# Optimization experiments

Measured on AMD Instinct MI355X. Metric: run time of the kernel, lower is better.

The kernel has to match this reference:

```python
import jax, jax.numpy as jnp
import numpy as np

L = 2        # num_layers
D = 512      # d_model
H = 8        # heads
C = 512      # GAT per-head out channels (= d_model, concat=False -> mean over heads)
B, S, E = 4, 512, 4096
NEG = jnp.float32(-1e9)


def setup_inputs() -> dict:
    key = jax.random.key(0)
    ks = jax.random.split(key, 20)
    sc = 0.02  # weight init scale
    inp = {
        'x': jax.random.normal(ks[0], (B, S, D), jnp.float32),
        'Wq': jax.random.normal(ks[1], (L, D, D), jnp.float32) * sc,
        'bq': jnp.zeros((L, D), jnp.float32),
        'Wk': jax.random.normal(ks[2], (L, D, D), jnp.float32) * sc,
        'bk': jnp.zeros((L, D), jnp.float32),
        'Wv': jax.random.normal(ks[3], (L, D, D), jnp.float32) * sc,
        'bv': jnp.zeros((L, D), jnp.float32),
        'Wo': jax.random.normal(ks[4], (L, D, D), jnp.float32) * sc,
        'bo': jnp.zeros((L, D), jnp.float32),
        'gatW': jax.random.normal(ks[5], (L, D, H * C), jnp.float32) * sc,
        'att_src': jax.random.normal(ks[6], (L, H, C), jnp.float32) * sc,
        'att_dst': jax.random.normal(ks[7], (L, H, C), jnp.float32) * sc,
        'gat_bias': jnp.zeros((L, C), jnp.float32),
        'ln_g': jnp.ones((L, D), jnp.float32),
        'ln_b': jnp.zeros((L, D), jnp.float32),
        'input_len': jax.random.randint(ks[8], (B,), S // 2, S + 1, jnp.int32),
        'edges': jax.random.randint(ks[9], (B, 2, E), 0, S // 2, jnp.int32),
        'edge_num': jax.random.randint(ks[10], (B,), E // 2, E + 1, jnp.int32),
    }
    return inp


def layer_norm(x, g, b, eps=1e-5):
    m = x.mean(-1, keepdims=True)
    v = ((x - m) ** 2).mean(-1, keepdims=True)
    return (x - m) * jax.lax.rsqrt(v + eps) * g + b


def mha(x, pad_mask, Wq, bq, Wk, bk, Wv, bv, Wo, bo):
    # pad_mask: [B,S] True where padded (masked out)
    b, s, d = x.shape
    dh = d // H
    q = (x @ Wq + bq).reshape(b, s, H, dh)
    k = (x @ Wk + bk).reshape(b, s, H, dh)
    v = (x @ Wv + bv).reshape(b, s, H, dh)
    scores = jnp.einsum('bqhd,bkhd->bhqk', q, k) / jnp.float32(np.sqrt(dh))
    scores = jnp.where(pad_mask[:, None, None, :], NEG, scores)
    a = jax.nn.softmax(scores, axis=-1)
    o = jnp.einsum('bhqk,bkhd->bqhd', a, v).reshape(b, s, d)
    return o @ Wo + bo


def gat_single(x, edge_index, edge_mask, node_mask, W, a_src_w, a_dst_w, bias):
    # x: [S,D]; edge_index: [2,E]; GATConv(d_model,d_model,heads,concat=False)
    s = x.shape[0]
    h = (x @ W).reshape(s, H, C)
    a_src_n = (h * a_src_w).sum(-1)  # [S,H]
    a_dst_n = (h * a_dst_w).sum(-1)  # [S,H]
    # add self loops (PyG default) for valid nodes
    ar = jnp.arange(s, dtype=edge_index.dtype)
    src = jnp.concatenate([edge_index[0], ar])
    dst = jnp.concatenate([edge_index[1], ar])
    em = jnp.concatenate([edge_mask, node_mask])  # [E+S]
    alpha = jax.nn.leaky_relu(a_src_n[src] + a_dst_n[dst], 0.2)  # [E+S,H]
    alpha = jnp.where(em[:, None], alpha, NEG)
    amax = jax.ops.segment_max(alpha, dst, num_segments=s)  # [S,H]
    ex = jnp.exp(alpha - amax[dst]) * em[:, None].astype(alpha.dtype)
    denom = jax.ops.segment_sum(ex, dst, num_segments=s)
    coef = ex / (denom[dst] + 1e-16)
    msg = h[src] * coef[:, :, None]  # [E+S,H,C]
    out = jax.ops.segment_sum(msg, dst, num_segments=s)  # [S,H,C]
    return out.mean(axis=1) + bias  # concat=False -> mean over heads


def reference(x, Wq, bq, Wk, bk, Wv, bv, Wo, bo, gatW, att_src, att_dst,
              gat_bias, ln_g, ln_b, input_len, edges, edge_num):
    b, s, d = x.shape
    node_mask = jnp.arange(s)[None, :] < input_len[:, None]      # [B,S]
    edge_mask = jnp.arange(edges.shape[-1])[None, :] < edge_num[:, None]  # [B,E]
    pad_mask = ~node_mask
    out = x
    layer_outputs = []
    gat_b = jax.vmap(gat_single, in_axes=(0, 0, 0, 0, None, None, None, None))
    for i in range(L):
        out = mha(out, pad_mask, Wq[i], bq[i], Wk[i], bk[i], Wv[i], bv[i], Wo[i], bo[i])
        g = gat_b(out, edges, edge_mask, node_mask,
                  gatW[i], att_src[i], att_dst[i], gat_bias[i])
        y = jax.nn.relu(layer_norm(g, ln_g[i], ln_b[i])) + out
        out = jnp.where(node_mask[:, :, None], y, out)
        layer_outputs.append(out)
    return jnp.stack(layer_outputs)  # [L,B,S,D]
```

## Files before the change

### kernel.cpp

```cpp
#include <hip/hip_runtime.h>
#include <cstddef>

#define DMODEL 512
#define HEADS  8
#define DH     64
#define CCH    512
#define BATCH  4
#define SEQ    512
#define NEDGE  4096
#define NLAYER 2
#define HC     (HEADS*CCH)

typedef unsigned short bf16_t;
typedef __attribute__((ext_vector_type(8))) short short8;
typedef __attribute__((ext_vector_type(4))) float floatx4;

__device__ __forceinline__ bf16_t f2bf(float f){
  unsigned u = __float_as_uint(f);
  unsigned r = (u + 0x7FFFu + ((u>>16)&1u)) >> 16;
  return (bf16_t)r;
}
__device__ __forceinline__ float bf2f(bf16_t u){ return __uint_as_float(((unsigned)u)<<16); }

__global__ void k_zero(int* __restrict__ p, int n){
  int i = blockIdx.x*256 + threadIdx.x;
  if (i < n) p[i] = 0;
}

__global__ void k_f2b(const float* __restrict__ in, bf16_t* __restrict__ out, int n4){
  int i = blockIdx.x*256 + threadIdx.x;
  if (i < n4){
    float4 v = ((const float4*)in)[i];
    ushort4 o;
    o.x=f2bf(v.x); o.y=f2bf(v.y); o.z=f2bf(v.z); o.w=f2bf(v.w);
    ((ushort4*)out)[i]=o;
  }
}

struct WtJob { const float* W[10]; bf16_t* WT[10]; };
__global__ __launch_bounds__(256) void k_wt_all(WtJob j){
  __shared__ float T[32][65];
  int t = blockIdx.x, k0 = blockIdx.y*32;
  int wsel, n0, N;
  if (t < 64){ wsel = t>>3; n0 = (t&7)*64; N = 512; }
  else { int t2 = t-64; wsel = 8 + (t2>>6); n0 = (t2&63)*64; N = 4096; }
  const float* W = j.W[wsel];
  bf16_t* WT = j.WT[wsel];
  const int K = 512;
  int tid = threadIdx.x;
  int lk = tid>>3, ln = (tid&7)*8;
  const float* src = W + (size_t)(k0+lk)*N + n0 + ln;
  float4 v0 = *(const float4*)src;
  float4 v1 = *(const float4*)(src+4);
  T[lk][ln+0]=v0.x; T[lk][ln+1]=v0.y; T[lk][ln+2]=v0.z; T[lk][ln+3]=v0.w;
  T[lk][ln+4]=v1.x; T[lk][ln+5]=v1.y; T[lk][ln+6]=v1.z; T[lk][ln+7]=v1.w;
  __syncthreads();
  int wn = tid>>2, wk = (tid&3)*8;
  ushort4 o0, o1;
  o0.x=f2bf(T[wk+0][wn]); o0.y=f2bf(T[wk+1][wn]); o0.z=f2bf(T[wk+2][wn]); o0.w=f2bf(T[wk+3][wn]);
  o1.x=f2bf(T[wk+4][wn]); o1.y=f2bf(T[wk+5][wn]); o1.z=f2bf(T[wk+6][wn]); o1.w=f2bf(T[wk+7][wn]);
  bf16_t* dst = WT + (size_t)(n0+wn)*K + k0 + wk;
  *(ushort4*)dst = o0;
  *(ushort4*)(dst+4) = o1;
}

struct GemmB {
  const bf16_t* W; const float* bias; float* C; bf16_t* Cb;
  const float* att_s; const float* att_d; float* asrc; float* adst;
};
struct GemmB3 { GemmB g[3]; };

template<int BM, int BN>
__global__ __launch_bounds__(256) void k_gemm_mfma(const bf16_t* __restrict__ A, GemmB3 p,
                                                   int N, int K){
  constexpr int MI = BM/32;
  constexpr int NJ = BN/32;
  constexpr int ACH = BM/64;
  constexpr int BCH = BN/64;
  const GemmB& g = p.g[blockIdx.z];
  const bf16_t* Wt  = g.W;
  const float* bias = g.bias;
  float* C          = g.C;
  bf16_t* Cb        = g.Cb;
  __shared__ __align__(16) bf16_t As[2][BM*40];
  __shared__ __align__(16) bf16_t Bs[2][BN*40];
  int bm = blockIdx.x*BM, bn = blockIdx.y*BN;
  int tid = threadIdx.x;
  int wave = tid>>6, lane = tid&63;
  int wy = wave>>1, wx = wave&1;
  int quad = lane>>4, l16 = lane&15;
  floatx4 acc[MI][NJ];
  #pragma unroll
  for (int i=0;i<MI;i++)
    #pragma unroll
    for (int j=0;j<NJ;j++) acc[i][j] = (floatx4){0.f,0.f,0.f,0.f};
  int sr = tid>>2;
  int sc = (tid&3)<<3;
  const bf16_t* Aptr = A  + (size_t)(bm+sr)*K + sc;
  const bf16_t* Bptr = Wt + (size_t)(bn+sr)*K + sc;
  uint4 av[ACH], bv[BCH];
  #pragma unroll
  for (int c=0;c<ACH;c++) av[c] = *(const uint4*)(Aptr + (size_t)c*64*K);
  #pragma unroll
  for (int c=0;c<BCH;c++) bv[c] = *(const uint4*)(Bptr + (size_t)c*64*K);
  #pragma unroll
  for (int c=0;c<ACH;c++) *(uint4*)(As[0] + (size_t)(sr+c*64)*40 + sc) = av[c];
  #pragma unroll
  for (int c=0;c<BCH;c++) *(uint4*)(Bs[0] + (size_t)(sr+c*64)*40 + sc) = bv[c];
  int nk = K>>5;
  for (int kk=0; kk<nk; kk++){
    __syncthreads();
    if (kk+1 < nk){
      int ko = (kk+1)<<5;
      #pragma unroll
      for (int c=0;c<ACH;c++) av[c] = *(const uint4*)(Aptr + (size_t)c*64*K + ko);
      #pragma unroll
      for (int c=0;c<BCH;c++) bv[c] = *(const uint4*)(Bptr + (size_t)c*64*K + ko);
    }
    const bf16_t* Ab = As[kk&1];
    const bf16_t* Bb = Bs[kk&1];
    short8 af[MI], bfr[NJ];
    #pragma unroll
    for (int i=0;i<MI;i++) af[i]  = *(const short8*)(Ab + (size_t)(wy*(BM/2)+i*16+l16)*40 + quad*8);
    #pragma unroll
    for (int j=0;j<NJ;j++) bfr[j] = *(const short8*)(Bb + (size_t)(wx*(BN/2)+j*16+l16)*40 + quad*8);
    #pragma unroll
    for (int i=0;i<MI;i++)
      #pragma unroll
      for (int j=0;j<NJ;j++)
        acc[i][j] = __builtin_amdgcn_mfma_f32_16x16x32_bf16(af[i], bfr[j], acc[i][j], 0,0,0);
    if (kk+1 < nk){
      bf16_t* Aw = As[(kk+1)&1];
      bf16_t* Bw = Bs[(kk+1)&1];
      #pragma unroll
      for (int c=0;c<ACH;c++) *(uint4*)(Aw + (size_t)(sr+c*64)*40 + sc) = av[c];
      #pragma unroll
      for (int c=0;c<BCH;c++) *(uint4*)(Bw + (size_t)(sr+c*64)*40 + sc) = bv[c];
    }
  }
  #pragma unroll
  for (int i=0;i<MI;i++){
    int row = bm + wy*(BM/2) + i*16 + quad*4;
    #pragma unroll
    for (int j=0;j<NJ;j++){
      int col = bn + wx*(BN/2) + j*16 + l16;
      float bi = bias ? bias[col] : 0.f;
      #pragma unroll
      for (int r=0;r<4;r++){
        float vvv = acc[i][j][r] + bi;
        if (C)  C[(size_t)(row+r)*N + col] = vvv;
        if (Cb) Cb[(size_t)(row+r)*N + col] = f2bf(vvv);
      }
    }
  }
  if (g.asrc){
    int colbase = bn + wx*(BN/2);
    int hidx = colbase >> 9;
    float aw_s[NJ], aw_d[NJ];
    #pragma unroll
    for (int j=0;j<NJ;j++){
      int col = colbase + j*16 + l16;
      aw_s[j] = g.att_s[col];
      aw_d[j] = g.att_d[col];
    }
    #pragma unroll
    for (int i=0;i<MI;i++){
      #pragma unroll
      for (int r=0;r<4;r++){
        float ps=0.f, pd=0.f;
        #pragma unroll
        for (int j=0;j<NJ;j++){ ps += acc[i][j][r]*aw_s[j]; pd += acc[i][j][r]*aw_d[j]; }
        #pragma unroll
        for (int m2=1;m2<16;m2<<=1){ ps += __shfl_xor(ps,m2); pd += __shfl_xor(pd,m2); }
        if (l16==0){
          int row = bm + wy*(BM/2) + i*16 + quad*4 + r;
          atomicAdd(&g.asrc[row*HEADS + hidx], ps);
          atomicAdd(&g.adst[row*HEADS + hidx], pd);
        }
      }
    }
  }
}

__global__ __launch_bounds__(256) void k_attn_flash(const bf16_t* __restrict__ q,
    const bf16_t* __restrict__ k, const bf16_t* __restrict__ v,
    const int* __restrict__ input_len, bf16_t* __restrict__ o){
  __shared__ __align__(16) bf16_t Kt[64*72];
  __shared__ __align__(16) bf16_t Vt[64*72];
  __shared__ __align__(16) bf16_t Pt[4][16*72];
  int q0 = blockIdx.x*64;
  int h  = blockIdx.y, b = blockIdx.z;
  int len = input_len[b];
  int tid = threadIdx.x;
  int w = tid>>6, lane = tid&63;
  int quad = lane>>4, l16 = lane&15;
  const bf16_t* qrow = q + ((size_t)(b*SEQ + q0 + w*16 + l16))*DMODEL + h*DH;
  short8 qa0 = *(const short8*)(qrow + quad*8);
  short8 qa1 = *(const short8*)(qrow + quad*8 + 32);
  int kr = tid>>2, kc = (tid&3)<<4;
  int vr = lane,   vc = w<<4;
  const bf16_t* kbase = k + ((size_t)(b*SEQ))*DMODEL + h*DH;
  const bf16_t* vbase = v + ((size_t)(b*SEQ))*DMODEL + h*DH;
  floatx4 oacc[4];
  #pragma unroll
  for (int dt=0;dt<4;dt++) oacc[dt] = (floatx4){0.f,0.f,0.f,0.f};
  float mrun[4], lrun[4];
  #pragma unroll
  for (int r=0;r<4;r++){ mrun[r]=-1e30f; lrun[r]=0.f; }
  for (int kt=0; kt<SEQ; kt+=64){
    if (kt >= len) break;
    uint4 kv0 = *(const uint4*)(kbase + (size_t)(kt+kr)*DMODEL + kc);
    uint4 kv1 = *(const uint4*)(kbase + (size_t)(kt+kr)*DMODEL + kc + 8);
    uint4 vv0 = *(const uint4*)(vbase + (size_t)(kt+vr)*DMODEL + vc);
    uint4 vv1 = *(const uint4*)(vbase + (size_t)(kt+vr)*DMODEL + vc + 8);
    __syncthreads();
    *(uint4*)(Kt + kr*72 + kc)     = kv0;
    *(uint4*)(Kt + kr*72 + kc + 8) = kv1;
    const ushort* vp0 = (const ushort*)&vv0;
    const ushort* vp1 = (const ushort*)&vv1;
    #pragma unroll
    for (int i2=0;i2<8;i2++) Vt[(vc+i2)*72 + vr]   = vp0[i2];
    #pragma unroll
    for (int i2=0;i2<8;i2++) Vt[(vc+8+i2)*72 + vr] = vp1[i2];
    __syncthreads();
    floatx4 sacc[4];
    #pragma unroll
    for (int nt=0;nt<4;nt++){
      sacc[nt] = (floatx4){0.f,0.f,0.f,0.f};
      short8 kb0 = *(const short8*)(Kt + (nt*16+l16)*72 + quad*8);
      short8 kb1 = *(const short8*)(Kt + (nt*16+l16)*72 + quad*8 + 32);
      sacc[nt] = __builtin_amdgcn_mfma_f32_16x16x32_bf16(qa0, kb0, sacc[nt], 0,0,0);
      sacc[nt] = __builtin_amdgcn_mfma_f32_16x16x32_bf16(qa1, kb1, sacc[nt], 0,0,0);
    }
    #pragma unroll
    for (int nt=0;nt<4;nt++){
      bool valid = (kt + nt*16 + l16) < len;
      #pragma unroll
      for (int r=0;r<4;r++){
        float sv = sacc[nt][r]*0.125f;
        sacc[nt][r] = valid ? sv : -1e30f;
      }
    }
    float alpha[4];
    #pragma unroll
    for (int r=0;r<4;r++){
      float mx = fmaxf(fmaxf(sacc[0][r],sacc[1][r]), fmaxf(sacc[2][r],sacc[3][r]));
      #pragma unroll
      for (int off=1; off<16; off<<=1) mx = fmaxf(mx, __shfl_xor(mx, off));
      float mn = fmaxf(mrun[r], mx);
      alpha[r] = __expf(mrun[r]-mn);
      mrun[r] = mn;
      float rs = 0.f;
      #pragma unroll
      for (int nt=0;nt<4;nt++){
        float pp = __expf(sacc[nt][r]-mn);
        sacc[nt][r] = pp; rs += pp;
      }
      #pragma unroll
      for (int off=1; off<16; off<<=1) rs += __shfl_xor(rs, off);
      lrun[r] = lrun[r]*alpha[r] + rs;
    }
    #pragma unroll
    for (int dt=0;dt<4;dt++)
      #pragma unroll
      for (int r=0;r<4;r++) oacc[dt][r] *= alpha[r];
    bf16_t* pw = Pt[w];
    #pragma unroll
    for (int nt=0;nt<4;nt++)
      #pragma unroll
      for (int r=0;r<4;r++) pw[(quad*4+r)*72 + nt*16 + l16] = f2bf(sacc[nt][r]);
    short8 pa0 = *(const short8*)(pw + l16*72 + quad*8);
    short8 pa1 = *(const short8*)(pw + l16*72 + quad*8 + 32);
    #pragma unroll
    for (int dt=0;dt<4;dt++){
      short8 vb0 = *(const short8*)(Vt + (dt*16+l16)*72 + quad*8);
      short8 vb1 = *(const short8*)(Vt + (dt*16+l16)*72 + quad*8 + 32);
      oacc[dt] = __builtin_amdgcn_mfma_f32_16x16x32_bf16(pa0, vb0, oacc[dt], 0,0,0);
      oacc[dt] = __builtin_amdgcn_mfma_f32_16x16x32_bf16(pa1, vb1, oacc[dt], 0,0,0);
    }
  }
  bf16_t* obase = o + ((size_t)(b*SEQ + q0 + w*16 + quad*4))*DMODEL + h*DH;
  #pragma unroll
  for (int r=0;r<4;r++){
    float invl = 1.f/lrun[r];
    #pragma unroll
    for (int dt=0;dt<4;dt++)
      obase[(size_t)r*DMODEL + dt*16 + l16] = f2bf(oacc[dt][r]*invl);
  }
}

__global__ void k_count(const int* __restrict__ edges, const int* __restrict__ edge_num, int* __restrict__ cnt){
  int b = blockIdx.y;
  int e = blockIdx.x*256 + threadIdx.x;
  if (e >= NEDGE || e >= edge_num[b]) return;
  int dst = edges[(size_t)b*2*NEDGE + NEDGE + e];
  atomicAdd(&cnt[b*SEQ + dst], 1);
}
__global__ void k_prefix(const int* __restrict__ cnt, int* __restrict__ offs, int* __restrict__ cursor){
  if (threadIdx.x==0){
    int b = blockIdx.x, acc=0;
    for (int s=0;s<SEQ;s++){ offs[b*SEQ+s]=acc; cursor[b*SEQ+s]=acc; acc+=cnt[b*SEQ+s]; }
  }
}
__global__ void k_fill(const int* __restrict__ edges, const int* __restrict__ edge_num,
                       int* __restrict__ cursor, int* __restrict__ elist){
  int b = blockIdx.y;
  int e = blockIdx.x*256 + threadIdx.x;
  if (e >= NEDGE || e >= edge_num[b]) return;
  int dst = edges[(size_t)b*2*NEDGE + NEDGE + e];
  int pos = atomicAdd(&cursor[b*SEQ + dst], 1);
  elist[(size_t)b*NEDGE + pos] = e;
}

__global__ __launch_bounds__(256) void k_gat_agg(const bf16_t* __restrict__ hbuf,
    const float* __restrict__ asrc, const float* __restrict__ adst,
    const int* __restrict__ offs, const int* __restrict__ cnt, const int* __restrict__ elist,
    const int* __restrict__ edges, const int* __restrict__ input_len,
    const float* __restrict__ gat_bias, float* __restrict__ gout){
  int s = blockIdx.x, b = blockIdx.y;
  if (s >= input_len[b]) return;
  __shared__ float amax_s[8], den_s[8], adl[8];
  __shared__ float cf[32][8];
  __shared__ int   cs[32];
  int tid = threadIdx.x;
  int n = cnt[b*SEQ+s];
  const int* el = elist + (size_t)b*NEDGE + offs[b*SEQ+s];
  const int* srcrow = edges + (size_t)b*2*NEDGE;
  if (tid < 8) adl[tid] = adst[(b*SEQ+s)*HEADS + tid];
  __syncthreads();
  if (tid < 64){
    float mx[8];
    #pragma unroll
    for (int h2=0;h2<8;h2++) mx[h2] = -1e30f;
    for (int j = tid; j <= n; j += 64){
      int src = (j==n) ? s : srcrow[el[j]];
      const float* ap = asrc + (size_t)(b*SEQ+src)*HEADS;
      #pragma unroll
      for (int h2=0;h2<8;h2++){
        float a = ap[h2] + adl[h2];
        a = (a>0.f)? a : 0.2f*a;
        mx[h2] = fmaxf(mx[h2], a);
      }
    }
    #pragma unroll
    for (int h2=0;h2<8;h2++){
      float vmx = mx[h2];
      #pragma unroll
      for (int off=32; off; off>>=1) vmx = fmaxf(vmx, __shfl_xor(vmx,off,64));
      mx[h2]=vmx;
    }
    float sm[8];
    #pragma unroll
    for (int h2=0;h2<8;h2++) sm[h2]=0.f;
    for (int j = tid; j <= n; j += 64){
      int src = (j==n) ? s : srcrow[el[j]];
      const float* ap = asrc + (size_t)(b*SEQ+src)*HEADS;
      #pragma unroll
      for (int h2=0;h2<8;h2++){
        float a = ap[h2] + adl[h2];
        a = (a>0.f)? a : 0.2f*a;
        sm[h2] += __expf(a - mx[h2]);
      }
    }
    #pragma unroll
    for (int h2=0;h2<8;h2++){
      float vs = sm[h2];
      #pragma unroll
      for (int off=32; off; off>>=1) vs += __shfl_xor(vs,off,64);
      if (tid==0){ amax_s[h2]=mx[h2]; den_s[h2]=vs; }
    }
  }
  __syncthreads();
  float acc0=0.f, acc1=0.f;
  int c0 = tid*2;
  for (int j0=0; j0 <= n; j0 += 32){
    int jm = min(32, n+1-j0);
    if (tid < jm*8){
      int jj = j0 + (tid>>3), h2 = tid&7;
      int src = (jj==n) ? s : srcrow[el[jj]];
      if (h2==0) cs[tid>>3] = src;
      float a = asrc[(size_t)(b*SEQ+src)*HEADS + h2] + adl[h2];
      a = (a>0.f)? a : 0.2f*a;
      cf[tid>>3][h2] = __expf(a - amax_s[h2]) / (den_s[h2] + 1e-16f);
    }
    __syncthreads();
    for (int jj=0; jj<jm; ++jj){
      int src = cs[jj];
      const bf16_t* hrow = hbuf + ((size_t)(b*SEQ+src))*HC;
      #pragma unroll
      for (int h2=0;h2<8;h2++){
        float wgt = cf[jj][h2];
        ushort2 hv = *(const ushort2*)(hrow + h2*CCH + c0);
        acc0 += wgt * bf2f(hv.x);
        acc1 += wgt * bf2f(hv.y);
      }
    }
    __syncthreads();
  }
  size_t gbse = ((size_t)(b*SEQ+s))*CCH;
  float2 outv = { acc0*0.125f + gat_bias[c0], acc1*0.125f + gat_bias[c0+1] };
  *(float2*)(gout + gbse + c0) = outv;
}

__global__ __launch_bounds__(256) void k_combine(const float* __restrict__ gbuf, const float* __restrict__ xin,
    const float* __restrict__ lng, const float* __restrict__ lnb,
    const int* __restrict__ input_len, bf16_t* __restrict__ curb, float* __restrict__ outp){
  __shared__ float red[256];
  int s = blockIdx.x, b = blockIdx.y, tid = threadIdx.x;
  size_t row = ((size_t)(b*SEQ+s))*DMODEL;
  float x0 = xin[row+tid], x1 = xin[row+tid+256];
  float y0 = x0, y1 = x1;
  if (s < input_len[b]){
    float g0 = gbuf[row+tid], g1 = gbuf[row+tid+256];
    red[tid] = g0+g1;
    __syncthreads();
    for (int off=128; off; off>>=1){ if (tid<off) red[tid]+=red[tid+off]; __syncthreads(); }
    float mean = red[0]*(1.f/512.f);
    __syncthreads();
    float d0 = g0-mean, d1 = g1-mean;
    red[tid] = d0*d0 + d1*d1;
    __syncthreads();
    for (int off=128; off; off>>=1){ if (tid<off) red[tid]+=red[tid+off]; __syncthreads(); }
    float inv = rsqrtf(red[0]*(1.f/512.f) + 1e-5f);
    float t0 = d0*inv*lng[tid]     + lnb[tid];
    float t1 = d1*inv*lng[tid+256] + lnb[tid+256];
    y0 = fmaxf(t0,0.f) + x0;
    y1 = fmaxf(t1,0.f) + x1;
  }
  curb[row+tid]=f2bf(y0); curb[row+tid+256]=f2bf(y1);
  outp[row+tid]=y0; outp[row+tid+256]=y1;
}

extern "C" void kernel_launch(void* const* d_in, const int* in_sizes, int n_in,
                              void* d_out, int out_size, void* d_ws, size_t ws_size,
                              hipStream_t stream){
  (void)in_sizes; (void)n_in; (void)out_size; (void)ws_size;
  const float* x       = (const float*)d_in[0];
  const float* Wq      = (const float*)d_in[1];
  const float* bq      = (const float*)d_in[2];
  const float* Wk      = (const float*)d_in[3];
  const float* bk      = (const float*)d_in[4];
  const float* Wv      = (const float*)d_in[5];
  const float* bv      = (const float*)d_in[6];
  const float* Wo      = (const float*)d_in[7];
  const float* bo      = (const float*)d_in[8];
  const float* gatW    = (const float*)d_in[9];
  const float* att_src = (const float*)d_in[10];
  const float* att_dst = (const float*)d_in[11];
  const float* gat_bias= (const float*)d_in[12];
  const float* ln_g    = (const float*)d_in[13];
  const float* ln_b    = (const float*)d_in[14];
  const int* input_len  = (const int*)d_in[15];
  const int* edges      = (const int*)d_in[16];
  const int* edge_num   = (const int*)d_in[17];
  float* outp = (float*)d_out;

  char* w = (char*)d_ws;
  size_t off = 0;
  auto alloc = [&](size_t bytes)->char*{ char* p = w + off; off += (bytes + 255) & ~(size_t)255; return p; };
  const size_t BSD = (size_t)BATCH*SEQ*DMODEL;
  const size_t BSH = (size_t)BATCH*SEQ*HEADS;
  float* mha  = (float*)alloc(BSD*4);
  bf16_t* hb  = (bf16_t*)alloc((size_t)BATCH*SEQ*HC*2);
  float* gb   = (float*)alloc(BSD*4);
  float* attn_nodes = (float*)alloc(2*BSH*4);
  float* asrc = attn_nodes;
  float* adst = attn_nodes + BSH;
  int* cnt    = (int*)alloc(BATCH*SEQ*4);
  int* offs   = (int*)alloc(BATCH*SEQ*4);
  int* cursor = (int*)alloc(BATCH*SEQ*4);
  int* elist  = (int*)alloc((size_t)BATCH*NEDGE*4);
  bf16_t* xbf  = (bf16_t*)alloc(BSD*2);
  bf16_t* curb = (bf16_t*)alloc(BSD*2);
  bf16_t* qbf  = (bf16_t*)alloc(BSD*2);
  bf16_t* kbf  = (bf16_t*)alloc(BSD*2);
  bf16_t* vbf  = (bf16_t*)alloc(BSD*2);
  bf16_t* obf  = (bf16_t*)alloc(BSD*2);
  bf16_t* abf  = (bf16_t*)alloc(BSD*2);
  bf16_t* wqt  = (bf16_t*)alloc((size_t)NLAYER*DMODEL*DMODEL*2);
  bf16_t* wkt  = (bf16_t*)alloc((size_t)NLAYER*DMODEL*DMODEL*2);
  bf16_t* wvt  = (bf16_t*)alloc((size_t)NLAYER*DMODEL*DMODEL*2);
  bf16_t* wot  = (bf16_t*)alloc((size_t)NLAYER*DMODEL*DMODEL*2);
  bf16_t* gwt  = (bf16_t*)alloc((size_t)NLAYER*DMODEL*HC*2);

  k_zero<<<dim3((BATCH*SEQ+255)/256),256,0,stream>>>(cnt, BATCH*SEQ);
  k_count<<<dim3(NEDGE/256, BATCH),256,0,stream>>>(edges, edge_num, cnt);
  k_prefix<<<dim3(BATCH),64,0,stream>>>(cnt, offs, cursor);
  k_fill<<<dim3(NEDGE/256, BATCH),256,0,stream>>>(edges, edge_num, cursor, elist);

  WtJob wj;
  for (int i=0;i<NLAYER;i++){
    size_t wo = (size_t)i*DMODEL*DMODEL;
    wj.W[i*4+0]=Wq+wo;  wj.WT[i*4+0]=wqt+wo;
    wj.W[i*4+1]=Wk+wo;  wj.WT[i*4+1]=wkt+wo;
    wj.W[i*4+2]=Wv+wo;  wj.WT[i*4+2]=wvt+wo;
    wj.W[i*4+3]=Wo+wo;  wj.WT[i*4+3]=wot+wo;
    size_t go = (size_t)i*DMODEL*HC;
    wj.W[8+i]=gatW+go;  wj.WT[8+i]=gwt+go;
  }
  k_wt_all<<<dim3(192, 16),256,0,stream>>>(wj);
  k_f2b<<<dim3((unsigned)(BSD/4/256)),256,0,stream>>>(x, xbf, (int)(BSD/4));

  const int M = BATCH*SEQ;
  for (int i=0;i<NLAYER;i++){
    size_t wo = (size_t)i*DMODEL*DMODEL;
    size_t bo2 = (size_t)i*DMODEL;
    const bf16_t* Ab = (i==0) ? xbf : curb;
    GemmB3 qkv;
    qkv.g[0] = { wqt+wo, bq+bo2, nullptr, qbf, nullptr, nullptr, nullptr, nullptr };
    qkv.g[1] = { wkt+wo, bk+bo2, nullptr, kbf, nullptr, nullptr, nullptr, nullptr };
    qkv.g[2] = { wvt+wo, bv+bo2, nullptr, vbf, nullptr, nullptr, nullptr, nullptr };
    k_gemm_mfma<64,64><<<dim3(M/64, DMODEL/64, 3),256,0,stream>>>(Ab, qkv, DMODEL, DMODEL);
    k_attn_flash<<<dim3(SEQ/64, HEADS, BATCH),256,0,stream>>>(qbf, kbf, vbf, input_len, obf);
    GemmB3 og;
    og.g[0] = { wot+wo, bo+bo2, mha, abf, nullptr, nullptr, nullptr, nullptr };
    og.g[1] = og.g[0]; og.g[2] = og.g[0];
    k_gemm_mfma<64,64><<<dim3(M/64, DMODEL/64, 1),256,0,stream>>>(obf, og, DMODEL, DMODEL);
    k_zero<<<dim3((unsigned)((2*BSH+255)/256)),256,0,stream>>>((int*)attn_nodes, (int)(2*BSH));
    GemmB3 gg;
    gg.g[0] = { gwt + (size_t)i*DMODEL*HC, nullptr, nullptr, hb,
                att_src + (size_t)i*HC, att_dst + (size_t)i*HC, asrc, adst };
    gg.g[1] = gg.g[0]; gg.g[2] = gg.g[0];
    k_gemm_mfma<64,64><<<dim3(M/64, HC/64, 1),256,0,stream>>>(abf, gg, HC, DMODEL);
    k_gat_agg<<<dim3(SEQ, BATCH),256,0,stream>>>(hb, asrc, adst, offs, cnt, elist, edges, input_len, gat_bias + (size_t)i*CCH, gb);
    k_combine<<<dim3(SEQ, BATCH),256,0,stream>>>(gb, mha, ln_g+bo2, ln_b+bo2, input_len, curb, outp + (size_t)i*BSD);
  }
}
```

Measured before the change: 331.1 us.

## Deepen GEMM global-load prefetch to three stages with register ring buffer

Replaces the single-stage register prefetch in the MFMA GEMM main loop with a four-slot register ring that keeps global loads three K-steps ahead, unrolling the K loop by four. The aim is to hide global memory latency better behind MFMA work. The cost is more vector registers held live, which may lower occupancy or cause spills. It also assumes K/32 is a multiple of four.

```diff
diff --git a/kernel.cpp b/kernel.cpp
--- a/kernel.cpp
+++ b/kernel.cpp
@@ -98,44 +98,53 @@
   int sc = (tid&3)<<3;
   const bf16_t* Aptr = A  + (size_t)(bm+sr)*K + sc;
   const bf16_t* Bptr = Wt + (size_t)(bn+sr)*K + sc;
-  uint4 av[ACH], bv[BCH];
-  #pragma unroll
-  for (int c=0;c<ACH;c++) av[c] = *(const uint4*)(Aptr + (size_t)c*64*K);
-  #pragma unroll
-  for (int c=0;c<BCH;c++) bv[c] = *(const uint4*)(Bptr + (size_t)c*64*K);
-  #pragma unroll
-  for (int c=0;c<ACH;c++) *(uint4*)(As[0] + (size_t)(sr+c*64)*40 + sc) = av[c];
-  #pragma unroll
-  for (int c=0;c<BCH;c++) *(uint4*)(Bs[0] + (size_t)(sr+c*64)*40 + sc) = bv[c];
-  int nk = K>>5;
-  for (int kk=0; kk<nk; kk++){
-    __syncthreads();
-    if (kk+1 < nk){
-      int ko = (kk+1)<<5;
-      #pragma unroll
-      for (int c=0;c<ACH;c++) av[c] = *(const uint4*)(Aptr + (size_t)c*64*K + ko);
-      #pragma unroll
-      for (int c=0;c<BCH;c++) bv[c] = *(const uint4*)(Bptr + (size_t)c*64*K + ko);
-    }
-    const bf16_t* Ab = As[kk&1];
-    const bf16_t* Bb = Bs[kk&1];
-    short8 af[MI], bfr[NJ];
-    #pragma unroll
-    for (int i=0;i<MI;i++) af[i]  = *(const short8*)(Ab + (size_t)(wy*(BM/2)+i*16+l16)*40 + quad*8);
-    #pragma unroll
-    for (int j=0;j<NJ;j++) bfr[j] = *(const short8*)(Bb + (size_t)(wx*(BN/2)+j*16+l16)*40 + quad*8);
-    #pragma unroll
-    for (int i=0;i<MI;i++)
-      #pragma unroll
-      for (int j=0;j<NJ;j++)
-        acc[i][j] = __builtin_amdgcn_mfma_f32_16x16x32_bf16(af[i], bfr[j], acc[i][j], 0,0,0);
-    if (kk+1 < nk){
-      bf16_t* Aw = As[(kk+1)&1];
-      bf16_t* Bw = Bs[(kk+1)&1];
-      #pragma unroll
-      for (int c=0;c<ACH;c++) *(uint4*)(Aw + (size_t)(sr+c*64)*40 + sc) = av[c];
-      #pragma unroll
-      for (int c=0;c<BCH;c++) *(uint4*)(Bw + (size_t)(sr+c*64)*40 + sc) = bv[c];
+  uint4 av[4][ACH], bv[4][BCH];
+  const int nk = K>>5;
+  #pragma unroll
+  for (int s=0;s<3;s++){
+    #pragma unroll
+    for (int c=0;c<ACH;c++) av[s][c] = *(const uint4*)(Aptr + (size_t)c*64*K + (s<<5));
+    #pragma unroll
+    for (int c=0;c<BCH;c++) bv[s][c] = *(const uint4*)(Bptr + (size_t)c*64*K + (s<<5));
+  }
+  #pragma unroll
+  for (int c=0;c<ACH;c++) *(uint4*)(As[0] + (size_t)(sr+c*64)*40 + sc) = av[0][c];
+  #pragma unroll
+  for (int c=0;c<BCH;c++) *(uint4*)(Bs[0] + (size_t)(sr+c*64)*40 + sc) = bv[0][c];
+  for (int kk=0; kk<nk; kk+=4){
+    #pragma unroll
+    for (int u=0;u<4;u++){
+      const int k = kk+u;
+      __syncthreads();
+      if (k+3 < nk){
+        const int qs = (u+3)&3;
+        const int ko = (k+3)<<5;
+        #pragma unroll
+        for (int c=0;c<ACH;c++) av[qs][c] = *(const uint4*)(Aptr + (size_t)c*64*K + ko);
+        #pragma unroll
+        for (int c=0;c<BCH;c++) bv[qs][c] = *(const uint4*)(Bptr + (size_t)c*64*K + ko);
+      }
+      const bf16_t* Ab = As[k&1];
+      const bf16_t* Bb = Bs[k&1];
+      short8 af[MI], bfr[NJ];
+      #pragma unroll
+      for (int i=0;i<MI;i++) af[i]  = *(const short8*)(Ab + (size_t)(wy*(BM/2)+i*16+l16)*40 + quad*8);
+      #pragma unroll
+      for (int j=0;j<NJ;j++) bfr[j] = *(const short8*)(Bb + (size_t)(wx*(BN/2)+j*16+l16)*40 + quad*8);
+      #pragma unroll
+      for (int i=0;i<MI;i++)
+        #pragma unroll
+        for (int j=0;j<NJ;j++)
+          acc[i][j] = __builtin_amdgcn_mfma_f32_16x16x32_bf16(af[i], bfr[j], acc[i][j], 0,0,0);
+      if (k+1 < nk){
+        const int qs = (u+1)&3;
+        bf16_t* Aw = As[(k+1)&1];
+        bf16_t* Bw = Bs[(k+1)&1];
+        #pragma unroll
+        for (int c=0;c<ACH;c++) *(uint4*)(Aw + (size_t)(sr+c*64)*40 + sc) = av[qs][c];
+        #pragma unroll
+        for (int c=0;c<BCH;c++) *(uint4*)(Bw + (size_t)(sr+c*64)*40 + sc) = bv[qs][c];
+      }
     }
   }
   #pragma unroll
```

After: 503.0 us. +51.9%, slower.
